# Kernel tuning notes

Hardware: AMD Instinct MI355X
Metric: run time of the kernel (lower is better)

## Reference

```python
import jax, jax.numpy as jnp
import numpy as np

EPS = 1e-6

def setup_inputs() -> dict:
    key = jax.random.key(0)
    ks = jax.random.split(key, 8)
    D = 64
    x = jax.random.normal(ks[0], (32, 56, 56, 4 * D), jnp.float32)
    beta = jnp.zeros((1, 1, 1, 4 * D), jnp.float32)
    diag = lambda k: 0.5 + 0.1 * jax.random.uniform(k, (D,), jnp.float32)
    off = lambda k: 0.05 * jax.random.normal(k, (D,), jnp.float32)
    k2 = jax.random.split(ks[1], 10)
    return dict(
        x=x, beta=beta,
        gam_rr=diag(k2[0]), gam_ri=off(k2[1]), gam_rj=off(k2[2]), gam_rk=off(k2[3]),
        gam_ii=diag(k2[4]), gam_ij=off(k2[5]), gam_ik=off(k2[6]),
        gam_jj=diag(k2[7]), gam_jk=off(k2[8]), gam_kk=diag(k2[9]),
    )

def _hbn(x, beta, gam_rr, gam_ri, gam_rj, gam_rk, gam_ii, gam_ij, gam_ik, gam_jj, gam_jk, gam_kk):
    # Training-mode quaternion/tessarine whitening BN (activation_position='after').
    N, H, W, C = x.shape
    d = C // 4
    mean = jnp.mean(x, axis=(0, 1, 2))           # [C]
    c = x - mean
    r, i, j, k = jnp.split(c, 4, axis=-1)        # each [N,H,W,d]
    m = lambda a, b: jnp.mean(a * b, axis=(0, 1, 2))  # [d]
    Vrr = m(r, r) + EPS; Vri = m(r, i); Vrj = m(r, j); Vrk = m(r, k)
    Vii = m(i, i) + EPS; Vij = m(i, j); Vik = m(i, k)
    Vjj = m(j, j) + EPS; Vjk = m(j, k); Vkk = m(k, k) + EPS
    # Symmetric 4x4 covariance per channel -> [d,4,4]
    V = jnp.stack([
        jnp.stack([Vrr, Vri, Vrj, Vrk], -1),
        jnp.stack([Vri, Vii, Vij, Vik], -1),
        jnp.stack([Vrj, Vij, Vjj, Vjk], -1),
        jnp.stack([Vrk, Vik, Vjk, Vkk], -1)], -2)
    # Whitening matrix W = V^{-1/2} (ZCA) via symmetric eigendecomposition
    w, U = jnp.linalg.eigh(V)
    Wm = jnp.einsum('dab,db,dcb->dac', U, 1.0 / jnp.sqrt(w), U)  # [d,4,4]
    v = jnp.stack([r, i, j, k], axis=-1)         # [N,H,W,d,4]
    xh = jnp.einsum('dec,nhwdc->nhwde', Wm, v)   # whitened components
    # 10-parameter symmetric affine recombination
    G = jnp.stack([
        jnp.stack([gam_rr, gam_ri, gam_rj, gam_rk], -1),
        jnp.stack([gam_ri, gam_ii, gam_ij, gam_ik], -1),
        jnp.stack([gam_rj, gam_ij, gam_jj, gam_jk], -1),
        jnp.stack([gam_rk, gam_ik, gam_jk, gam_kk], -1)], -2)  # [d,4,4]
    y = jnp.einsum('dec,nhwdc->nhwde', G, xh)
    y = jnp.concatenate([y[..., 0], y[..., 1], y[..., 2], y[..., 3]], axis=-1) + beta
    return jax.nn.elu(y)

def reference(x, beta, gam_rr, gam_ri, gam_rj, gam_rk, gam_ii, gam_ij, gam_ik, gam_jj, gam_jk, gam_kk):
    return _hbn(x, beta, gam_rr, gam_ri, gam_rj, gam_rk, gam_ii, gam_ij, gam_ik, gam_jj, gam_jk, gam_kk)
```

## Files before the change

kernel.cpp:

```cpp
#include <hip/hip_runtime.h>
#include <math.h>

static constexpr int NPOS = 32 * 56 * 56;
static constexpr int CCH  = 256;
static constexpr double EPSV = 1e-6;

__global__ __launch_bounds__(256) void hbn_reduce(const float* __restrict__ x,
                                                  double* __restrict__ S) {
  const int tid  = threadIdx.x;
  const int lane = tid & 63;
  const int gw   = blockIdx.x * (blockDim.x >> 6) + (tid >> 6);
  const int nw   = gridDim.x * (blockDim.x >> 6);

  float s0=0.f, s1=0.f, s2=0.f, s3=0.f;
  float q0=0.f,q1=0.f,q2=0.f,q3=0.f,q4=0.f,q5=0.f,q6=0.f,q7=0.f,q8=0.f,q9=0.f;

  for (int p = gw * 2; p < NPOS; p += nw * 2) {
    const float* b = x + (size_t)p * CCH + lane;
    float r0 = b[0],   i0 = b[64],  j0 = b[128], k0 = b[192];
    float r1 = b[256], i1 = b[320], j1 = b[384], k1 = b[448];
    s0 += r0 + r1; s1 += i0 + i1; s2 += j0 + j1; s3 += k0 + k1;
    q0 = fmaf(r0,r0, fmaf(r1,r1, q0));
    q1 = fmaf(r0,i0, fmaf(r1,i1, q1));
    q2 = fmaf(r0,j0, fmaf(r1,j1, q2));
    q3 = fmaf(r0,k0, fmaf(r1,k1, q3));
    q4 = fmaf(i0,i0, fmaf(i1,i1, q4));
    q5 = fmaf(i0,j0, fmaf(i1,j1, q5));
    q6 = fmaf(i0,k0, fmaf(i1,k1, q6));
    q7 = fmaf(j0,j0, fmaf(j1,j1, q7));
    q8 = fmaf(j0,k0, fmaf(j1,k1, q8));
    q9 = fmaf(k0,k0, fmaf(k1,k1, q9));
  }

  __shared__ float red[14][256];
  red[0][tid]=s0;  red[1][tid]=s1;  red[2][tid]=s2;  red[3][tid]=s3;
  red[4][tid]=q0;  red[5][tid]=q1;  red[6][tid]=q2;  red[7][tid]=q3;
  red[8][tid]=q4;  red[9][tid]=q5;  red[10][tid]=q6; red[11][tid]=q7;
  red[12][tid]=q8; red[13][tid]=q9;
  __syncthreads();
  if (tid < 64) {
#pragma unroll
    for (int q = 0; q < 14; ++q) {
      double v = (double)red[q][tid] + (double)red[q][tid+64]
               + (double)red[q][tid+128] + (double)red[q][tid+192];
      unsafeAtomicAdd(&S[q*64 + tid], v);
    }
  }
}

__global__ void hbn_solve(const double* __restrict__ S,
                          const float* __restrict__ beta,
                          const float* __restrict__ grr, const float* __restrict__ gri,
                          const float* __restrict__ grj, const float* __restrict__ grk,
                          const float* __restrict__ gii, const float* __restrict__ gij,
                          const float* __restrict__ gik, const float* __restrict__ gjj,
                          const float* __restrict__ gjk, const float* __restrict__ gkk,
                          float* __restrict__ Mmat, float* __restrict__ offv) {
  const int d = threadIdx.x;
  const double invM = 1.0 / (double)NPOS;

  double mu[4];
  mu[0] = S[0*64+d]*invM; mu[1] = S[1*64+d]*invM;
  mu[2] = S[2*64+d]*invM; mu[3] = S[3*64+d]*invM;

  double A[4][4];
  A[0][0] = S[4*64+d]*invM  - mu[0]*mu[0] + EPSV;
  A[0][1] = A[1][0] = S[5*64+d]*invM  - mu[0]*mu[1];
  A[0][2] = A[2][0] = S[6*64+d]*invM  - mu[0]*mu[2];
  A[0][3] = A[3][0] = S[7*64+d]*invM  - mu[0]*mu[3];
  A[1][1] = S[8*64+d]*invM  - mu[1]*mu[1] + EPSV;
  A[1][2] = A[2][1] = S[9*64+d]*invM  - mu[1]*mu[2];
  A[1][3] = A[3][1] = S[10*64+d]*invM - mu[1]*mu[3];
  A[2][2] = S[11*64+d]*invM - mu[2]*mu[2] + EPSV;
  A[2][3] = A[3][2] = S[12*64+d]*invM - mu[2]*mu[3];
  A[3][3] = S[13*64+d]*invM - mu[3]*mu[3] + EPSV;

  double U[4][4] = {{1,0,0,0},{0,1,0,0},{0,0,1,0},{0,0,0,1}};

#pragma unroll 1
  for (int sweep = 0; sweep < 8; ++sweep) {
#pragma unroll
    for (int p = 0; p < 3; ++p) {
#pragma unroll
      for (int q = p + 1; q < 4; ++q) {
        double apq = A[p][q];
        if (fabs(apq) > 1e-300) {
          double theta = (A[q][q] - A[p][p]) / (2.0 * apq);
          double t = 1.0 / (fabs(theta) + sqrt(theta*theta + 1.0));
          if (theta < 0.0) t = -t;
          double c = 1.0 / sqrt(t*t + 1.0);
          double s = t * c;
#pragma unroll
          for (int r = 0; r < 4; ++r) {
            double arp = A[r][p], arq = A[r][q];
            A[r][p] = c*arp - s*arq;  A[r][q] = s*arp + c*arq;
          }
#pragma unroll
          for (int r = 0; r < 4; ++r) {
            double apr = A[p][r], aqr = A[q][r];
            A[p][r] = c*apr - s*aqr;  A[q][r] = s*apr + c*aqr;
          }
#pragma unroll
          for (int r = 0; r < 4; ++r) {
            double urp = U[r][p], urq = U[r][q];
            U[r][p] = c*urp - s*urq;  U[r][q] = s*urp + c*urq;
          }
        }
      }
    }
  }

  double wis[4];
#pragma unroll
  for (int b = 0; b < 4; ++b) {
    double w = A[b][b];
    if (w < 1e-12) w = 1e-12;
    wis[b] = 1.0 / sqrt(w);
  }

  double Wm[4][4];
#pragma unroll
  for (int a = 0; a < 4; ++a)
#pragma unroll
    for (int cc = 0; cc < 4; ++cc) {
      double acc = 0.0;
#pragma unroll
      for (int b = 0; b < 4; ++b) acc += U[a][b] * wis[b] * U[cc][b];
      Wm[a][cc] = acc;
    }

  double G[4][4];
  G[0][0] = grr[d]; G[0][1] = G[1][0] = gri[d];
  G[0][2] = G[2][0] = grj[d]; G[0][3] = G[3][0] = grk[d];
  G[1][1] = gii[d]; G[1][2] = G[2][1] = gij[d];
  G[1][3] = G[3][1] = gik[d];
  G[2][2] = gjj[d]; G[2][3] = G[3][2] = gjk[d];
  G[3][3] = gkk[d];

  double M[4][4];
#pragma unroll
  for (int e = 0; e < 4; ++e)
#pragma unroll
    for (int cc = 0; cc < 4; ++cc) {
      double acc = 0.0;
#pragma unroll
      for (int b = 0; b < 4; ++b) acc += G[e][b] * Wm[b][cc];
      M[e][cc] = acc;
      Mmat[d*16 + e*4 + cc] = (float)acc;
    }

#pragma unroll
  for (int e = 0; e < 4; ++e) {
    double acc = (double)beta[e*64 + d];
#pragma unroll
    for (int cc = 0; cc < 4; ++cc) acc -= M[e][cc] * mu[cc];
    offv[e*64 + d] = (float)acc;
  }
}

__global__ __launch_bounds__(256) void hbn_apply(const float* __restrict__ x,
                                                 const float* __restrict__ Mmat,
                                                 const float* __restrict__ offv,
                                                 float* __restrict__ out) {
  const int tid  = threadIdx.x;
  const int lane = tid & 63;
  const int gw   = blockIdx.x * (blockDim.x >> 6) + (tid >> 6);
  const int nw   = gridDim.x * (blockDim.x >> 6);

  float m0  = Mmat[lane*16+0],  m1  = Mmat[lane*16+1],  m2  = Mmat[lane*16+2],  m3  = Mmat[lane*16+3];
  float m4  = Mmat[lane*16+4],  m5  = Mmat[lane*16+5],  m6  = Mmat[lane*16+6],  m7  = Mmat[lane*16+7];
  float m8  = Mmat[lane*16+8],  m9  = Mmat[lane*16+9],  m10 = Mmat[lane*16+10], m11 = Mmat[lane*16+11];
  float m12 = Mmat[lane*16+12], m13 = Mmat[lane*16+13], m14 = Mmat[lane*16+14], m15 = Mmat[lane*16+15];
  const float o0 = offv[lane], o1 = offv[64+lane], o2 = offv[128+lane], o3 = offv[192+lane];

  for (int p = gw * 2; p < NPOS; p += nw * 2) {
    const float* b = x + (size_t)p * CCH + lane;
    float r0 = b[0],   i0 = b[64],  j0 = b[128], k0 = b[192];
    float r1 = b[256], i1 = b[320], j1 = b[384], k1 = b[448];

    float ya0 = fmaf(m0, r0, fmaf(m1, i0, fmaf(m2, j0, fmaf(m3, k0, o0))));
    float ya1 = fmaf(m4, r0, fmaf(m5, i0, fmaf(m6, j0, fmaf(m7, k0, o1))));
    float ya2 = fmaf(m8, r0, fmaf(m9, i0, fmaf(m10,j0, fmaf(m11,k0, o2))));
    float ya3 = fmaf(m12,r0, fmaf(m13,i0, fmaf(m14,j0, fmaf(m15,k0, o3))));
    float yb0 = fmaf(m0, r1, fmaf(m1, i1, fmaf(m2, j1, fmaf(m3, k1, o0))));
    float yb1 = fmaf(m4, r1, fmaf(m5, i1, fmaf(m6, j1, fmaf(m7, k1, o1))));
    float yb2 = fmaf(m8, r1, fmaf(m9, i1, fmaf(m10,j1, fmaf(m11,k1, o2))));
    float yb3 = fmaf(m12,r1, fmaf(m13,i1, fmaf(m14,j1, fmaf(m15,k1, o3))));

    ya0 = ya0 > 0.f ? ya0 : (__expf(ya0) - 1.f);
    ya1 = ya1 > 0.f ? ya1 : (__expf(ya1) - 1.f);
    ya2 = ya2 > 0.f ? ya2 : (__expf(ya2) - 1.f);
    ya3 = ya3 > 0.f ? ya3 : (__expf(ya3) - 1.f);
    yb0 = yb0 > 0.f ? yb0 : (__expf(yb0) - 1.f);
    yb1 = yb1 > 0.f ? yb1 : (__expf(yb1) - 1.f);
    yb2 = yb2 > 0.f ? yb2 : (__expf(yb2) - 1.f);
    yb3 = yb3 > 0.f ? yb3 : (__expf(yb3) - 1.f);

    float* ob = out + (size_t)p * CCH + lane;
    ob[0]   = ya0; ob[64]  = ya1; ob[128] = ya2; ob[192] = ya3;
    ob[256] = yb0; ob[320] = yb1; ob[384] = yb2; ob[448] = yb3;
  }
}

extern "C" void kernel_launch(void* const* d_in, const int* in_sizes, int n_in,
                              void* d_out, int out_size, void* d_ws, size_t ws_size,
                              hipStream_t stream) {
  (void)in_sizes; (void)n_in; (void)out_size; (void)ws_size;
  const float* x    = (const float*)d_in[0];
  const float* beta = (const float*)d_in[1];
  const float* grr  = (const float*)d_in[2];
  const float* gri  = (const float*)d_in[3];
  const float* grj  = (const float*)d_in[4];
  const float* grk  = (const float*)d_in[5];
  const float* gii  = (const float*)d_in[6];
  const float* gij  = (const float*)d_in[7];
  const float* gik  = (const float*)d_in[8];
  const float* gjj  = (const float*)d_in[9];
  const float* gjk  = (const float*)d_in[10];
  const float* gkk  = (const float*)d_in[11];
  float* out = (float*)d_out;

  double* S   = (double*)d_ws;
  float* Mmat = (float*)((char*)d_ws + 14*64*sizeof(double));
  float* offv = (float*)((char*)d_ws + 14*64*sizeof(double) + 64*16*sizeof(float));

  hipMemsetAsync(d_ws, 0, 14*64*sizeof(double), stream);
  hbn_reduce<<<512, 256, 0, stream>>>(x, S);
  hbn_solve<<<1, 64, 0, stream>>>(S, beta, grr, gri, grj, grk,
                                  gii, gij, gik, gjj, gjk, gkk, Mmat, offv);
  hbn_apply<<<1024, 256, 0, stream>>>(x, Mmat, offv, out);
}
```

Measured before the change: 83.57 us.

## Solve whitening in fp32, use nontemporal output stores, and enlarge grids

Converts the per-channel Jacobi eigen-solve and whitening-matrix construction from double to float with rsqrtf and fewer sweeps. The apply kernel now writes output with nontemporal stores to reduce cache pollution. Both the reduce and apply kernels are launched with more blocks to raise memory-level parallelism. The fp32 solve risks some loss of accuracy on ill-conditioned covariances, and the larger reduce grid adds more global atomics.

```diff
diff --git a/kernel.cpp b/kernel.cpp
--- a/kernel.cpp
+++ b/kernel.cpp
@@ -63,46 +63,46 @@
   mu[0] = S[0*64+d]*invM; mu[1] = S[1*64+d]*invM;
   mu[2] = S[2*64+d]*invM; mu[3] = S[3*64+d]*invM;
 
-  double A[4][4];
-  A[0][0] = S[4*64+d]*invM  - mu[0]*mu[0] + EPSV;
-  A[0][1] = A[1][0] = S[5*64+d]*invM  - mu[0]*mu[1];
-  A[0][2] = A[2][0] = S[6*64+d]*invM  - mu[0]*mu[2];
-  A[0][3] = A[3][0] = S[7*64+d]*invM  - mu[0]*mu[3];
-  A[1][1] = S[8*64+d]*invM  - mu[1]*mu[1] + EPSV;
-  A[1][2] = A[2][1] = S[9*64+d]*invM  - mu[1]*mu[2];
-  A[1][3] = A[3][1] = S[10*64+d]*invM - mu[1]*mu[3];
-  A[2][2] = S[11*64+d]*invM - mu[2]*mu[2] + EPSV;
-  A[2][3] = A[3][2] = S[12*64+d]*invM - mu[2]*mu[3];
-  A[3][3] = S[13*64+d]*invM - mu[3]*mu[3] + EPSV;
-
-  double U[4][4] = {{1,0,0,0},{0,1,0,0},{0,0,1,0},{0,0,0,1}};
+  float A[4][4];
+  A[0][0] = (float)(S[4*64+d]*invM  - mu[0]*mu[0] + EPSV);
+  A[0][1] = A[1][0] = (float)(S[5*64+d]*invM  - mu[0]*mu[1]);
+  A[0][2] = A[2][0] = (float)(S[6*64+d]*invM  - mu[0]*mu[2]);
+  A[0][3] = A[3][0] = (float)(S[7*64+d]*invM  - mu[0]*mu[3]);
+  A[1][1] = (float)(S[8*64+d]*invM  - mu[1]*mu[1] + EPSV);
+  A[1][2] = A[2][1] = (float)(S[9*64+d]*invM  - mu[1]*mu[2]);
+  A[1][3] = A[3][1] = (float)(S[10*64+d]*invM - mu[1]*mu[3]);
+  A[2][2] = (float)(S[11*64+d]*invM - mu[2]*mu[2] + EPSV);
+  A[2][3] = A[3][2] = (float)(S[12*64+d]*invM - mu[2]*mu[3]);
+  A[3][3] = (float)(S[13*64+d]*invM - mu[3]*mu[3] + EPSV);
+
+  float U[4][4] = {{1,0,0,0},{0,1,0,0},{0,0,1,0},{0,0,0,1}};
 
 #pragma unroll 1
-  for (int sweep = 0; sweep < 8; ++sweep) {
+  for (int sweep = 0; sweep < 6; ++sweep) {
 #pragma unroll
     for (int p = 0; p < 3; ++p) {
 #pragma unroll
       for (int q = p + 1; q < 4; ++q) {
-        double apq = A[p][q];
-        if (fabs(apq) > 1e-300) {
-          double theta = (A[q][q] - A[p][p]) / (2.0 * apq);
-          double t = 1.0 / (fabs(theta) + sqrt(theta*theta + 1.0));
-          if (theta < 0.0) t = -t;
-          double c = 1.0 / sqrt(t*t + 1.0);
-          double s = t * c;
+        float apq = A[p][q];
+        if (fabsf(apq) > 1e-30f) {
+          float theta = (A[q][q] - A[p][p]) / (2.0f * apq);
+          float t = 1.0f / (fabsf(theta) + sqrtf(fmaf(theta, theta, 1.0f)));
+          if (theta < 0.0f) t = -t;
+          float c = rsqrtf(fmaf(t, t, 1.0f));
+          float s = t * c;
 #pragma unroll
           for (int r = 0; r < 4; ++r) {
-            double arp = A[r][p], arq = A[r][q];
+            float arp = A[r][p], arq = A[r][q];
             A[r][p] = c*arp - s*arq;  A[r][q] = s*arp + c*arq;
           }
 #pragma unroll
           for (int r = 0; r < 4; ++r) {
-            double apr = A[p][r], aqr = A[q][r];
+            float apr = A[p][r], aqr = A[q][r];
             A[p][r] = c*apr - s*aqr;  A[q][r] = s*apr + c*aqr;
           }
 #pragma unroll
           for (int r = 0; r < 4; ++r) {
-            double urp = U[r][p], urq = U[r][q];
+            float urp = U[r][p], urq = U[r][q];
             U[r][p] = c*urp - s*urq;  U[r][q] = s*urp + c*urq;
           }
         }
@@ -110,26 +110,26 @@
     }
   }
 
-  double wis[4];
+  float wis[4];
 #pragma unroll
   for (int b = 0; b < 4; ++b) {
-    double w = A[b][b];
-    if (w < 1e-12) w = 1e-12;
-    wis[b] = 1.0 / sqrt(w);
-  }
-
-  double Wm[4][4];
+    float w = A[b][b];
+    if (w < 1e-12f) w = 1e-12f;
+    wis[b] = rsqrtf(w);
+  }
+
+  float Wm[4][4];
 #pragma unroll
   for (int a = 0; a < 4; ++a)
 #pragma unroll
     for (int cc = 0; cc < 4; ++cc) {
-      double acc = 0.0;
+      float acc = 0.0f;
 #pragma unroll
       for (int b = 0; b < 4; ++b) acc += U[a][b] * wis[b] * U[cc][b];
       Wm[a][cc] = acc;
     }
 
-  double G[4][4];
+  float G[4][4];
   G[0][0] = grr[d]; G[0][1] = G[1][0] = gri[d];
   G[0][2] = G[2][0] = grj[d]; G[0][3] = G[3][0] = grk[d];
   G[1][1] = gii[d]; G[1][2] = G[2][1] = gij[d];
@@ -137,24 +137,24 @@
   G[2][2] = gjj[d]; G[2][3] = G[3][2] = gjk[d];
   G[3][3] = gkk[d];
 
-  double M[4][4];
+  float M[4][4];
 #pragma unroll
   for (int e = 0; e < 4; ++e)
 #pragma unroll
     for (int cc = 0; cc < 4; ++cc) {
-      double acc = 0.0;
+      float acc = 0.0f;
 #pragma unroll
       for (int b = 0; b < 4; ++b) acc += G[e][b] * Wm[b][cc];
       M[e][cc] = acc;
-      Mmat[d*16 + e*4 + cc] = (float)acc;
+      Mmat[d*16 + e*4 + cc] = acc;
     }
 
 #pragma unroll
   for (int e = 0; e < 4; ++e) {
-    double acc = (double)beta[e*64 + d];
-#pragma unroll
-    for (int cc = 0; cc < 4; ++cc) acc -= M[e][cc] * mu[cc];
-    offv[e*64 + d] = (float)acc;
+    float acc = beta[e*64 + d];
+#pragma unroll
+    for (int cc = 0; cc < 4; ++cc) acc -= M[e][cc] * (float)mu[cc];
+    offv[e*64 + d] = acc;
   }
 }
 
@@ -167,10 +167,10 @@
   const int gw   = blockIdx.x * (blockDim.x >> 6) + (tid >> 6);
   const int nw   = gridDim.x * (blockDim.x >> 6);
 
-  float m0  = Mmat[lane*16+0],  m1  = Mmat[lane*16+1],  m2  = Mmat[lane*16+2],  m3  = Mmat[lane*16+3];
-  float m4  = Mmat[lane*16+4],  m5  = Mmat[lane*16+5],  m6  = Mmat[lane*16+6],  m7  = Mmat[lane*16+7];
-  float m8  = Mmat[lane*16+8],  m9  = Mmat[lane*16+9],  m10 = Mmat[lane*16+10], m11 = Mmat[lane*16+11];
-  float m12 = Mmat[lane*16+12], m13 = Mmat[lane*16+13], m14 = Mmat[lane*16+14], m15 = Mmat[lane*16+15];
+  const float m0  = Mmat[lane*16+0],  m1  = Mmat[lane*16+1],  m2  = Mmat[lane*16+2],  m3  = Mmat[lane*16+3];
+  const float m4  = Mmat[lane*16+4],  m5  = Mmat[lane*16+5],  m6  = Mmat[lane*16+6],  m7  = Mmat[lane*16+7];
+  const float m8  = Mmat[lane*16+8],  m9  = Mmat[lane*16+9],  m10 = Mmat[lane*16+10], m11 = Mmat[lane*16+11];
+  const float m12 = Mmat[lane*16+12], m13 = Mmat[lane*16+13], m14 = Mmat[lane*16+14], m15 = Mmat[lane*16+15];
   const float o0 = offv[lane], o1 = offv[64+lane], o2 = offv[128+lane], o3 = offv[192+lane];
 
   for (int p = gw * 2; p < NPOS; p += nw * 2) {
@@ -197,8 +197,14 @@
     yb3 = yb3 > 0.f ? yb3 : (__expf(yb3) - 1.f);
 
     float* ob = out + (size_t)p * CCH + lane;
-    ob[0]   = ya0; ob[64]  = ya1; ob[128] = ya2; ob[192] = ya3;
-    ob[256] = yb0; ob[320] = yb1; ob[384] = yb2; ob[448] = yb3;
+    __builtin_nontemporal_store(ya0, ob + 0);
+    __builtin_nontemporal_store(ya1, ob + 64);
+    __builtin_nontemporal_store(ya2, ob + 128);
+    __builtin_nontemporal_store(ya3, ob + 192);
+    __builtin_nontemporal_store(yb0, ob + 256);
+    __builtin_nontemporal_store(yb1, ob + 320);
+    __builtin_nontemporal_store(yb2, ob + 384);
+    __builtin_nontemporal_store(yb3, ob + 448);
   }
 }
 
@@ -225,8 +231,8 @@
   float* offv = (float*)((char*)d_ws + 14*64*sizeof(double) + 64*16*sizeof(float));
 
   hipMemsetAsync(d_ws, 0, 14*64*sizeof(double), stream);
-  hbn_reduce<<<512, 256, 0, stream>>>(x, S);
+  hbn_reduce<<<2048, 256, 0, stream>>>(x, S);
   hbn_solve<<<1, 64, 0, stream>>>(S, beta, grr, gri, grj, grk,
                                   gii, gij, gik, gjj, gjk, gkk, Mmat, offv);
-  hbn_apply<<<1024, 256, 0, stream>>>(x, Mmat, offv, out);
-}
+  hbn_apply<<<2048, 256, 0, stream>>>(x, Mmat, offv, out);
+}
```

Measured after the change: 109.6 us. 31.1% more time.
